# Kernel optimization log

Measured on AMD Instinct MI355X. Metric: run time of the kernel, lower is better.

The kernel has to match this reference:

```python
import jax, jax.numpy as jnp
import numpy as np

N, NDIM, K, M = 65536, 512, 512, 200


def setup_inputs() -> dict:
    key = jax.random.key(0)
    k1, k2, k3, k4, k5 = jax.random.split(key, 5)
    data = jax.random.normal(k1, (N, NDIM), dtype=jnp.float32)
    # Orthogonal projection A, as in __init__: QR of randn with sign fix
    A0 = np.asarray(jax.random.normal(k2, (NDIM, K), dtype=jnp.float32), dtype=np.float64)
    Q, R = np.linalg.qr(A0)
    A = jnp.asarray(Q * np.sign(np.diag(R)), dtype=jnp.float32)
    # Monotonic knot grids on roughly [-4, 4] with M knots per direction
    span = 8.0 / (M - 1)
    dx = jax.random.uniform(k3, (K, M - 1), minval=0.5 * span, maxval=1.5 * span)
    xx = jnp.concatenate([jnp.full((K, 1), -4.0), -4.0 + jnp.cumsum(dx, axis=1)], axis=1).astype(jnp.float32)
    dy = jax.random.uniform(k4, (K, M - 1), minval=0.5 * span, maxval=1.5 * span)
    yy = jnp.concatenate([jnp.full((K, 1), -4.0), -4.0 + jnp.cumsum(dy, axis=1)], axis=1).astype(jnp.float32)
    delta = jax.random.uniform(k5, (K, M), minval=0.5, maxval=2.0, dtype=jnp.float32)
    return {"data": data, "A": A, "xx": xx, "yy": yy, "delta": delta}


def _rq_spline_forward(x, xx, yy, delta):
    """Monotonic rational-quadratic spline, applied per dimension.
    x: (N, K) values; xx, yy, delta: (K, M) knot positions / values / derivatives.
    Returns (y, log|dy/dx|), both (N, K).
    """
    Mk = xx.shape[1]
    # Per-dimension bin search: idx in [0, Mk]
    idx = jax.vmap(jnp.searchsorted, in_axes=(0, 1))(xx, x).T  # (N, K)
    below = idx == 0
    above = idx == Mk
    b = jnp.clip(idx, 1, Mk - 1) - 1  # interior bin index, (N, K)
    bt = b.T  # (K, N) for take_along_axis on (K, M) tables
    g = lambda t, o: jnp.take_along_axis(t, bt + o, axis=1).T  # -> (N, K)
    xk, xk1 = g(xx, 0), g(xx, 1)
    yk, yk1 = g(yy, 0), g(yy, 1)
    dk, dk1 = g(delta, 0), g(delta, 1)
    dx = xk1 - xk
    dy = yk1 - yk
    s = dy / dx  # bin slope
    xi = jnp.clip((x - xk) / dx, 0.0, 1.0)  # clipped so out-of-range pts stay finite
    xi1 = 1.0 - xi
    denom = s + (dk1 + dk - 2.0 * s) * xi * xi1
    y_in = yk + dy * (s * xi * xi + dk * xi * xi1) / denom
    logd_in = (2.0 * jnp.log(s)
               + jnp.log(dk1 * xi * xi + 2.0 * s * xi * xi1 + dk * xi1 * xi1)
               - 2.0 * jnp.log(denom))
    # Linear extrapolation outside the knot range with endpoint derivatives
    x0, xN_ = xx[:, 0], xx[:, -1]
    y0, yN_ = yy[:, 0], yy[:, -1]
    d0, dN_ = delta[:, 0], delta[:, -1]
    y = jnp.where(below, y0 + d0 * (x - x0),
                  jnp.where(above, yN_ + dN_ * (x - xN_), y_in))
    logd = jnp.where(below, jnp.log(d0),
                     jnp.where(above, jnp.log(dN_), logd_in))
    return y, logd


def reference(data, A, xx, yy, delta):
    data0 = data @ A                    # (N, K) sliced projection
    remaining = data - data0 @ A.T      # component orthogonal to the slices
    y, logd = _rq_spline_forward(data0, xx, yy, delta)
    logj = jnp.sum(logd, axis=1)        # (N,) log-Jacobian
    out = remaining + y @ A.T
    return out, logj
```

## Files before the change

### kernel.cpp

```cpp
#include <hip/hip_runtime.h>

#define N_ROWS 65536
#define DIM 512
#define MKNOTS 200
#define KT 16
#define NCHUNK 2048
#define NCELL 768

typedef _Float16 f16x8 __attribute__((ext_vector_type(8)));
typedef _Float16 f16x4 __attribute__((ext_vector_type(4)));
typedef float f32x4 __attribute__((ext_vector_type(4)));

__device__ inline void gload16(const void* g, void* l) {
  __builtin_amdgcn_global_load_lds(
      (const __attribute__((address_space(1))) void*)g,
      (__attribute__((address_space(3))) void*)l,
      16, 0, 0);
}

template <bool S3, bool ADDSRC>
__global__ __launch_bounds__(256)
void gemm_k(const _Float16* __restrict__ Ah, const _Float16* __restrict__ Al,
            const _Float16* __restrict__ Bth, const _Float16* __restrict__ Btl,
            const float* __restrict__ addsrc, float* __restrict__ C)
{
  __shared__ alignas(16) _Float16 smem[S3 ? 16384 : 8192];
  _Float16* sAh = smem;
  _Float16* sBh = smem + 4096;
  _Float16* sAl = S3 ? smem + 8192  : smem;
  _Float16* sBl = S3 ? smem + 12288 : smem;

  const int tid  = threadIdx.x;
  const int bm   = blockIdx.x * 128;
  const int bn   = blockIdx.y * 128;
  const int wm   = ((tid >> 6) >> 1) * 64;
  const int wn   = ((tid >> 6) & 1) * 64;
  const int lane = tid & 63;
  const int lm   = lane & 15;
  const int quad = lane >> 4;
  const int sr   = tid >> 2;
  const int sc   = (tid & 3) * 8;

  const _Float16* gAh = Ah  + (size_t)(bm + sr) * DIM + sc;
  const _Float16* gBh = Bth + (size_t)(bn + sr) * DIM + sc;
  const _Float16* gAl = S3 ? (Al  + (size_t)(bm + sr) * DIM + sc) : gAh;
  const _Float16* gBl = S3 ? (Btl + (size_t)(bn + sr) * DIM + sc) : gBh;

  f32x4 acc[4][4] = {};

  for (int k0 = 0; k0 < DIM; k0 += 32) {
    gload16(gAh + k0,               sAh + tid * 8);
    gload16(gAh + k0 + 64 * DIM,    sAh + 2048 + tid * 8);
    gload16(gBh + k0,               sBh + tid * 8);
    gload16(gBh + k0 + 64 * DIM,    sBh + 2048 + tid * 8);
    if constexpr (S3) {
      gload16(gAl + k0,             sAl + tid * 8);
      gload16(gAl + k0 + 64 * DIM,  sAl + 2048 + tid * 8);
      gload16(gBl + k0,             sBl + tid * 8);
      gload16(gBl + k0 + 64 * DIM,  sBl + 2048 + tid * 8);
    }
    __syncthreads();

    f16x8 a_h[4], b_h[4], a_l[4], b_l[4];
    #pragma unroll
    for (int i = 0; i < 4; ++i) {
      a_h[i] = *(const f16x8*)&sAh[(wm + i * 16 + lm) * 32 + quad * 8];
      b_h[i] = *(const f16x8*)&sBh[(wn + i * 16 + lm) * 32 + quad * 8];
      if constexpr (S3) {
        a_l[i] = *(const f16x8*)&sAl[(wm + i * 16 + lm) * 32 + quad * 8];
        b_l[i] = *(const f16x8*)&sBl[(wn + i * 16 + lm) * 32 + quad * 8];
      }
    }
    #pragma unroll
    for (int i = 0; i < 4; ++i)
      #pragma unroll
      for (int j = 0; j < 4; ++j) {
        acc[i][j] = __builtin_amdgcn_mfma_f32_16x16x32_f16(a_h[i], b_h[j], acc[i][j], 0, 0, 0);
        if constexpr (S3) {
          acc[i][j] = __builtin_amdgcn_mfma_f32_16x16x32_f16(a_h[i], b_l[j], acc[i][j], 0, 0, 0);
          acc[i][j] = __builtin_amdgcn_mfma_f32_16x16x32_f16(a_l[i], b_h[j], acc[i][j], 0, 0, 0);
        }
      }
    __syncthreads();
  }

  #pragma unroll
  for (int i = 0; i < 4; ++i)
    #pragma unroll
    for (int j = 0; j < 4; ++j)
      #pragma unroll
      for (int r = 0; r < 4; ++r) {
        const int row = bm + wm + i * 16 + quad * 4 + r;
        const int col = bn + wn + j * 16 + lm;
        const size_t idx = (size_t)row * DIM + col;
        float v = acc[i][j][r];
        if constexpr (ADDSRC) v += addsrc[idx];
        C[idx] = v;
      }
}

__global__ __launch_bounds__(256)
void conv_data_k(const float* __restrict__ in, _Float16* __restrict__ hi,
                 _Float16* __restrict__ lo)
{
  const size_t i = ((size_t)blockIdx.x * 256 + threadIdx.x) * 4;
  const float4 v = *reinterpret_cast<const float4*>(in + i);
  f16x4 h, l;
  h.x = (_Float16)v.x; l.x = (_Float16)(v.x - (float)h.x);
  h.y = (_Float16)v.y; l.y = (_Float16)(v.y - (float)h.y);
  h.z = (_Float16)v.z; l.z = (_Float16)(v.z - (float)h.z);
  h.w = (_Float16)v.w; l.w = (_Float16)(v.w - (float)h.w);
  *reinterpret_cast<f16x4*>(hi + i) = h;
  *reinterpret_cast<f16x4*>(lo + i) = l;
}

__global__ __launch_bounds__(256)
void conv_A_k(const float* __restrict__ A, _Float16* __restrict__ Ah,
              _Float16* __restrict__ Al, _Float16* __restrict__ ATh,
              _Float16* __restrict__ ATl)
{
  const int i = blockIdx.x * 256 + threadIdx.x;
  const int r = i >> 9, c = i & 511;
  const float v = A[i];
  const _Float16 h = (_Float16)v;
  const _Float16 l = (_Float16)(v - (float)h);
  Ah[i] = h; Al[i] = l;
  ATh[c * 512 + r] = h; ATl[c * 512 + r] = l;
}

__global__ __launch_bounds__(256)
void prep_k(const float* __restrict__ xx, const float* __restrict__ yy,
            const float* __restrict__ dd, float4* __restrict__ pkG,
            unsigned char* __restrict__ bucketG)
{
  __shared__ float xr[MKNOTS], yr[MKNOTS];
  const int k = blockIdx.x, tid = threadIdx.x;
  if (tid < MKNOTS) {
    xr[tid] = xx[k * MKNOTS + tid];
    yr[tid] = yy[k * MKNOTS + tid];
  }
  __syncthreads();
  if (tid < MKNOTS) {
    const float x0 = xr[tid], y0 = yr[tid], d0 = dd[k * MKNOTS + tid];
    float s = 0.f;
    if (tid < MKNOTS - 1) s = (yr[tid + 1] - y0) / (xr[tid + 1] - x0);
    pkG[k * MKNOTS + tid] = float4{x0, y0, d0, s};
  }
  for (int c = tid; c < NCELL; c += 256) {
    const float cl = -4.f + (float)c * 0.015625f;
    int lo = 0, hi = MKNOTS;
    while (lo < hi) { const int mid = (lo + hi) >> 1; if (xr[mid] <= cl) lo = mid + 1; else hi = mid; }
    bucketG[k * NCELL + c] = (unsigned char)lo;
  }
}

__global__ __launch_bounds__(512)
void spline_k(const float* __restrict__ data0, const float4* __restrict__ pkG,
              const unsigned char* __restrict__ bucketG,
              _Float16* __restrict__ zH, float* __restrict__ logj)
{
  __shared__ float4 sPK[KT * (MKNOTS + 1)];
  __shared__ unsigned int sBkt32[KT * 193];

  const int kBase = blockIdx.x * KT;
  const int nBase = blockIdx.y * NCHUNK;
  const int tid = threadIdx.x;

  for (int i = tid; i < KT * MKNOTS; i += 512) {
    const int r = i / MKNOTS, c = i - r * MKNOTS;
    sPK[r * (MKNOTS + 1) + c] = pkG[(kBase + r) * MKNOTS + c];
  }
  const unsigned int* bG32 = (const unsigned int*)bucketG;
  for (int i = tid; i < KT * (NCELL / 4); i += 512) {
    const int r = i / (NCELL / 4), c = i - r * (NCELL / 4);
    sBkt32[r * 193 + c] = bG32[(kBase + r) * (NCELL / 4) + c];
  }
  __syncthreads();

  const int kl = tid & 15;
  const int nl = tid >> 4;
  const float4* prow = sPK + kl * (MKNOTS + 1);
  const unsigned char* brow = (const unsigned char*)sBkt32 + kl * 772;

  #pragma unroll 2
  for (int nn = nl; nn < NCHUNK; nn += 32) {
    const int n = nBase + nn;
    const size_t gi = (size_t)n * DIM + kBase + kl;
    const float x = data0[gi];

    int idx;
    if (x <= -4.f) {
      idx = 0;
    } else {
      int c = (int)((x + 4.f) * 64.f);
      c = min(c, NCELL - 1);
      const int cnt0 = (int)brow[c];
      const int p = min(cnt0, MKNOTS - 1);
      const float xp = ((const float*)(prow + p))[0];
      idx = cnt0 + ((cnt0 <= MKNOTS - 1 && xp < x) ? 1 : 0);
    }
    const bool below = (idx == 0);
    const bool above = (idx >= MKNOTS);
    const int b = min(max(idx - 1, 0), MKNOTS - 2);

    const float4 pa = prow[b];
    const float4 pb = prow[b + 1];

    const float dxk = pb.x - pa.x;
    float xi = (x - pa.x) * __builtin_amdgcn_rcpf(dxk);
    xi = fminf(fmaxf(xi, 0.f), 1.f);
    const float xi1 = 1.f - xi;
    const float t = pa.w;
    const float g = xi * xi1;
    const float den = t + (pb.z + pa.z - 2.f * t) * g;
    const float rden = __builtin_amdgcn_rcpf(den);
    const float ynum = t * xi * xi + pa.z * g;
    float y = pa.y + t * dxk * ynum * rden;
    const float dnum = pb.z * xi * xi + 2.f * t * g + pa.z * xi1 * xi1;
    float logd = __logf(t * t * dnum * rden * rden);

    if (below) { y = pa.y + pa.z * (x - pa.x); logd = __logf(pa.z); }
    if (above) { y = pb.y + pb.z * (x - pb.x); logd = __logf(pb.z); }

    zH[gi] = (_Float16)(y - x);

    float v = logd;
    v += __shfl_xor(v, 8, 64);
    v += __shfl_xor(v, 4, 64);
    v += __shfl_xor(v, 2, 64);
    v += __shfl_xor(v, 1, 64);
    if (kl == 0) atomicAdd(&logj[n], v);
  }
}

extern "C" void kernel_launch(void* const* d_in, const int* in_sizes, int n_in,
                              void* d_out, int out_size, void* d_ws, size_t ws_size,
                              hipStream_t stream)
{
  const float* data  = (const float*)d_in[0];
  const float* A     = (const float*)d_in[1];
  const float* xx    = (const float*)d_in[2];
  const float* yy    = (const float*)d_in[3];
  const float* delta = (const float*)d_in[4];

  float* out  = (float*)d_out;
  float* logj = out + (size_t)N_ROWS * DIM;

  _Float16* dHi = (_Float16*)d_ws;
  _Float16* dLo = dHi + (size_t)N_ROWS * DIM;
  _Float16* Ah  = dLo + (size_t)N_ROWS * DIM;
  _Float16* Al  = Ah + 512 * 512;
  _Float16* ATh = Al + 512 * 512;
  _Float16* ATl = ATh + 512 * 512;
  float* data0  = (float*)(ATl + 512 * 512);
  _Float16* zH  = dHi;
  float4* pkG = (float4*)dLo;
  unsigned char* bucketG = (unsigned char*)(pkG + 512 * MKNOTS);

  conv_A_k<<<1024, 256, 0, stream>>>(A, Ah, Al, ATh, ATl);
  conv_data_k<<<(N_ROWS * DIM) / (256 * 4), 256, 0, stream>>>(data, dHi, dLo);

  gemm_k<true, false><<<dim3(N_ROWS / 128, DIM / 128), 256, 0, stream>>>(
      dHi, dLo, ATh, ATl, nullptr, data0);

  prep_k<<<512, 256, 0, stream>>>(xx, yy, delta, pkG, bucketG);
  hipMemsetAsync(logj, 0, N_ROWS * sizeof(float), stream);

  spline_k<<<dim3(DIM / KT, N_ROWS / NCHUNK), 512, 0, stream>>>(
      data0, pkG, bucketG, zH, logj);

  gemm_k<false, true><<<dim3(N_ROWS / 128, DIM / 128), 256, 0, stream>>>(
      zH, nullptr, Ah, nullptr, data, out);
}
```

Before: 647.7 us.

## Restructure spline kernel to one thread per row with vector loads and prefetch

The spline kernel moves from 16 threads per row (one per dimension, with shuffle reductions) to one thread per row that handles 16 dimensions. It loads each row slice as four float4 vectors, prefetches the next row, writes the outputs as two f16x8 stores, and issues one atomic per row with no shuffles. The bin lookup is reworked so the probed knot is reused as one endpoint, and NCHUNK doubles. The aim is to cut scalar global accesses, shuffle reductions and atomics. The cost is higher register pressure, and each thread's 16 dimensions read from different shared-memory rows, which may cause bank conflicts.

```diff
diff --git a/kernel.cpp b/kernel.cpp
--- a/kernel.cpp
+++ b/kernel.cpp
@@ -4,7 +4,7 @@
 #define DIM 512
 #define MKNOTS 200
 #define KT 16
-#define NCHUNK 2048
+#define NCHUNK 4096
 #define NCELL 768
 
 typedef _Float16 f16x8 __attribute__((ext_vector_type(8)));
@@ -154,7 +154,7 @@
   }
 }
 
-__global__ __launch_bounds__(512)
+__global__ __launch_bounds__(512, 4)
 void spline_k(const float* __restrict__ data0, const float4* __restrict__ pkG,
               const unsigned char* __restrict__ bucketG,
               _Float16* __restrict__ zH, float* __restrict__ logj)
@@ -177,59 +177,72 @@
   }
   __syncthreads();
 
-  const int kl = tid & 15;
-  const int nl = tid >> 4;
-  const float4* prow = sPK + kl * (MKNOTS + 1);
-  const unsigned char* brow = (const unsigned char*)sBkt32 + kl * 772;
-
-  #pragma unroll 2
-  for (int nn = nl; nn < NCHUNK; nn += 32) {
-    const int n = nBase + nn;
-    const size_t gi = (size_t)n * DIM + kBase + kl;
-    const float x = data0[gi];
-
-    int idx;
-    if (x <= -4.f) {
-      idx = 0;
-    } else {
-      int c = (int)((x + 4.f) * 64.f);
-      c = min(c, NCELL - 1);
-      const int cnt0 = (int)brow[c];
+  float4 cur[4], nxt[4];
+  {
+    const float4* p4 = (const float4*)(data0 + (size_t)(nBase + tid) * DIM + kBase);
+    #pragma unroll
+    for (int q = 0; q < 4; ++q) cur[q] = p4[q];
+  }
+
+  for (int it = 0; it < NCHUNK / 512; ++it) {
+    const int n = nBase + it * 512 + tid;
+    if (it + 1 < NCHUNK / 512) {
+      const float4* p4 = (const float4*)(data0 + (size_t)(n + 512) * DIM + kBase);
+      #pragma unroll
+      for (int q = 0; q < 4; ++q) nxt[q] = p4[q];
+    }
+
+    float acc = 0.f;
+    f16x8 z0, z1;
+    #pragma unroll
+    for (int j = 0; j < 16; ++j) {
+      const float x = ((const float*)cur)[j];
+      const float4* prow = sPK + j * (MKNOTS + 1);
+      const unsigned char* brow = (const unsigned char*)sBkt32 + j * 772;
+
+      int cnt0 = 0;
+      if (x > -4.f) {
+        int c = (int)((x + 4.f) * 64.f);
+        c = min(c, NCELL - 1);
+        cnt0 = (int)brow[c];
+      }
       const int p = min(cnt0, MKNOTS - 1);
-      const float xp = ((const float*)(prow + p))[0];
-      idx = cnt0 + ((cnt0 <= MKNOTS - 1 && xp < x) ? 1 : 0);
-    }
-    const bool below = (idx == 0);
-    const bool above = (idx >= MKNOTS);
-    const int b = min(max(idx - 1, 0), MKNOTS - 2);
-
-    const float4 pa = prow[b];
-    const float4 pb = prow[b + 1];
-
-    const float dxk = pb.x - pa.x;
-    float xi = (x - pa.x) * __builtin_amdgcn_rcpf(dxk);
-    xi = fminf(fmaxf(xi, 0.f), 1.f);
-    const float xi1 = 1.f - xi;
-    const float t = pa.w;
-    const float g = xi * xi1;
-    const float den = t + (pb.z + pa.z - 2.f * t) * g;
-    const float rden = __builtin_amdgcn_rcpf(den);
-    const float ynum = t * xi * xi + pa.z * g;
-    float y = pa.y + t * dxk * ynum * rden;
-    const float dnum = pb.z * xi * xi + 2.f * t * g + pa.z * xi1 * xi1;
-    float logd = __logf(t * t * dnum * rden * rden);
-
-    if (below) { y = pa.y + pa.z * (x - pa.x); logd = __logf(pa.z); }
-    if (above) { y = pb.y + pb.z * (x - pb.x); logd = __logf(pb.z); }
-
-    zH[gi] = (_Float16)(y - x);
-
-    float v = logd;
-    v += __shfl_xor(v, 8, 64);
-    v += __shfl_xor(v, 4, 64);
-    v += __shfl_xor(v, 2, 64);
-    v += __shfl_xor(v, 1, 64);
-    if (kl == 0) atomicAdd(&logj[n], v);
+      const float4 P = prow[p];
+      const bool take = (cnt0 <= MKNOTS - 1) && (P.x < x);
+      const int idx = cnt0 + (take ? 1 : 0);
+      const int qi = min(max(take ? p + 1 : p - 1, 0), MKNOTS - 1);
+      const float4 Q = prow[qi];
+      const bool edge = (idx == 0) || (idx >= MKNOTS);
+      const float4 pa = take ? P : Q;
+      const float4 pb = take ? Q : P;
+
+      const float dxk = pb.x - pa.x;
+      float xi = (x - pa.x) * __builtin_amdgcn_rcpf(dxk);
+      xi = fminf(fmaxf(xi, 0.f), 1.f);
+      const float xi1 = 1.f - xi;
+      const float t = pa.w;
+      const float g = xi * xi1;
+      const float den = t + (pb.z + pa.z - 2.f * t) * g;
+      const float rden = __builtin_amdgcn_rcpf(den);
+      float y = pa.y + t * dxk * (t * xi * xi + pa.z * g) * rden;
+      const float dnum = pb.z * xi * xi + 2.f * t * g + pa.z * xi1 * xi1;
+      float logd = __logf(t * t * dnum * rden * rden);
+      if (edge) {
+        y = P.y + P.z * (x - P.x);
+        logd = __logf(P.z);
+      }
+      acc += logd;
+      const _Float16 zz = (_Float16)(y - x);
+      if (j < 8) z0[j] = zz; else z1[j - 8] = zz;
+    }
+
+    _Float16* zp = zH + (size_t)n * DIM + kBase;
+    *(f16x8*)zp = z0;
+    *((f16x8*)zp + 1) = z1;
+    atomicAdd(&logj[n], acc);
+
+    #pragma unroll
+    for (int q = 0; q < 4; ++q) cur[q] = nxt[q];
   }
 }
 
```

After: 798.8 us. 23.3% more time.

## Restructure spline kernel: transposed row tiles, SoA knot tables, partial-sum logj reduction

Applied to the files above, without the earlier changes.

The spline kernel now maps one thread per row. Each thread processes 16 dimensions from a tile staged in LDS, and the z results are packed as fp16 pairs and written back cooperatively in coalesced form. Knot tables move from float4 AoS to separate x/y arrays plus fp16 derivatives, and the bucket grid is coarsened to 384 cells with a 2-step linear refine. Per-row atomics on logj are replaced by per-k-group partial sums written to workspace and then summed by a new reduce kernel. Storing derivatives in fp16 reduces precision in the logd and y computation, and bucket lookups now read global memory instead of LDS.

```diff
diff --git a/kernel.cpp b/kernel.cpp
--- a/kernel.cpp
+++ b/kernel.cpp
@@ -4,8 +4,9 @@
 #define DIM 512
 #define MKNOTS 200
 #define KT 16
-#define NCHUNK 2048
-#define NCELL 768
+#define NCELL 384
+#define TILE 256
+#define TPB 4
 
 typedef _Float16 f16x8 __attribute__((ext_vector_type(8)));
 typedef _Float16 f16x4 __attribute__((ext_vector_type(4)));
@@ -147,90 +148,124 @@
     pkG[k * MKNOTS + tid] = float4{x0, y0, d0, s};
   }
   for (int c = tid; c < NCELL; c += 256) {
-    const float cl = -4.f + (float)c * 0.015625f;
+    const float cl = -4.f + (float)c * 0.03125f;
     int lo = 0, hi = MKNOTS;
     while (lo < hi) { const int mid = (lo + hi) >> 1; if (xr[mid] <= cl) lo = mid + 1; else hi = mid; }
     bucketG[k * NCELL + c] = (unsigned char)lo;
   }
 }
 
-__global__ __launch_bounds__(512)
+__global__ __launch_bounds__(256)
 void spline_k(const float* __restrict__ data0, const float4* __restrict__ pkG,
               const unsigned char* __restrict__ bucketG,
-              _Float16* __restrict__ zH, float* __restrict__ logj)
-{
-  __shared__ float4 sPK[KT * (MKNOTS + 1)];
-  __shared__ unsigned int sBkt32[KT * 193];
+              _Float16* __restrict__ zH, float* __restrict__ ppart)
+{
+  __shared__ float sX[KT * 201];
+  __shared__ float sY[KT * 201];
+  __shared__ _Float16 sD[KT * 201 + 2];
+  __shared__ float xT[TILE * 17];
 
   const int kBase = blockIdx.x * KT;
-  const int nBase = blockIdx.y * NCHUNK;
+  const int nBase = blockIdx.y * (TILE * TPB);
   const int tid = threadIdx.x;
 
-  for (int i = tid; i < KT * MKNOTS; i += 512) {
+  for (int i = tid; i < KT * MKNOTS; i += 256) {
     const int r = i / MKNOTS, c = i - r * MKNOTS;
-    sPK[r * (MKNOTS + 1) + c] = pkG[(kBase + r) * MKNOTS + c];
-  }
-  const unsigned int* bG32 = (const unsigned int*)bucketG;
-  for (int i = tid; i < KT * (NCELL / 4); i += 512) {
-    const int r = i / (NCELL / 4), c = i - r * (NCELL / 4);
-    sBkt32[r * 193 + c] = bG32[(kBase + r) * (NCELL / 4) + c];
+    const float4 v = pkG[(kBase + r) * MKNOTS + c];
+    sX[r * 201 + c] = v.x;
+    sY[r * 201 + c] = v.y;
+    sD[r * 201 + c] = (_Float16)v.z;
   }
   __syncthreads();
 
-  const int kl = tid & 15;
-  const int nl = tid >> 4;
-  const float4* prow = sPK + kl * (MKNOTS + 1);
-  const unsigned char* brow = (const unsigned char*)sBkt32 + kl * 772;
-
-  #pragma unroll 2
-  for (int nn = nl; nn < NCHUNK; nn += 32) {
-    const int n = nBase + nn;
-    const size_t gi = (size_t)n * DIM + kBase + kl;
-    const float x = data0[gi];
-
-    int idx;
-    if (x <= -4.f) {
-      idx = 0;
-    } else {
-      int c = (int)((x + 4.f) * 64.f);
-      c = min(c, NCELL - 1);
-      const int cnt0 = (int)brow[c];
-      const int p = min(cnt0, MKNOTS - 1);
-      const float xp = ((const float*)(prow + p))[0];
-      idx = cnt0 + ((cnt0 <= MKNOTS - 1 && xp < x) ? 1 : 0);
-    }
-    const bool below = (idx == 0);
-    const bool above = (idx >= MKNOTS);
-    const int b = min(max(idx - 1, 0), MKNOTS - 2);
-
-    const float4 pa = prow[b];
-    const float4 pb = prow[b + 1];
-
-    const float dxk = pb.x - pa.x;
-    float xi = (x - pa.x) * __builtin_amdgcn_rcpf(dxk);
-    xi = fminf(fmaxf(xi, 0.f), 1.f);
-    const float xi1 = 1.f - xi;
-    const float t = pa.w;
-    const float g = xi * xi1;
-    const float den = t + (pb.z + pa.z - 2.f * t) * g;
-    const float rden = __builtin_amdgcn_rcpf(den);
-    const float ynum = t * xi * xi + pa.z * g;
-    float y = pa.y + t * dxk * ynum * rden;
-    const float dnum = pb.z * xi * xi + 2.f * t * g + pa.z * xi1 * xi1;
-    float logd = __logf(t * t * dnum * rden * rden);
-
-    if (below) { y = pa.y + pa.z * (x - pa.x); logd = __logf(pa.z); }
-    if (above) { y = pb.y + pb.z * (x - pb.x); logd = __logf(pb.z); }
-
-    zH[gi] = (_Float16)(y - x);
-
-    float v = logd;
-    v += __shfl_xor(v, 8, 64);
-    v += __shfl_xor(v, 4, 64);
-    v += __shfl_xor(v, 2, 64);
-    v += __shfl_xor(v, 1, 64);
-    if (kl == 0) atomicAdd(&logj[n], v);
-  }
+  for (int tile = 0; tile < TPB; ++tile) {
+    const int n0 = nBase + tile * TILE;
+
+    #pragma unroll
+    for (int rr = 0; rr < 4; ++rr) {
+      const int r = rr * 64 + (tid >> 2);
+      const float4 v = *((const float4*)(data0 + (size_t)(n0 + r) * DIM + kBase) + (tid & 3));
+      float* dst = &xT[r * 17 + (tid & 3) * 4];
+      dst[0] = v.x; dst[1] = v.y; dst[2] = v.z; dst[3] = v.w;
+    }
+    __syncthreads();
+
+    float acc = 0.f;
+    float zprev = 0.f;
+    #pragma unroll 4
+    for (int j = 0; j < KT; ++j) {
+      const float x = xT[tid * 17 + j];
+
+      int c = (int)((x + 4.f) * 32.f);
+      c = min(max(c, 0), NCELL - 1);
+      const int cnt0 = (int)bucketG[(kBase + j) * NCELL + c];
+
+      const int p = min(cnt0, MKNOTS - 2);
+      const int q0 = p - 1;
+      const float* rx = &sX[j * 201];
+      const float xm = rx[q0], x0 = rx[q0 + 1], x1 = rx[q0 + 2], x2 = rx[q0 + 3];
+      const int t2 = (x0 < x ? 1 : 0) + (x1 < x ? 1 : 0);
+      const int idx = p + t2;
+      const bool below = (x <= -4.f);
+      const bool above = (idx >= MKNOTS);
+      const int b = idx - 1;
+
+      const float xk  = (t2 == 0) ? xm : ((t2 == 1) ? x0 : x1);
+      const float xk1 = (t2 == 0) ? x0 : ((t2 == 1) ? x1 : x2);
+      const float yk  = sY[j * 201 + b];
+      const float yk1 = sY[j * 201 + b + 1];
+      const float dk  = (float)sD[j * 201 + b];
+      const float dk1 = (float)sD[j * 201 + b + 1];
+
+      const float dxk = xk1 - xk;
+      const float rdx = __builtin_amdgcn_rcpf(dxk);
+      const float s   = (yk1 - yk) * rdx;
+      float xi = (x - xk) * rdx;
+      xi = fminf(fmaxf(xi, 0.f), 1.f);
+      const float xi1 = 1.f - xi;
+      const float g = xi * xi1;
+      const float den = s + (dk1 + dk - 2.f * s) * g;
+      const float rden = __builtin_amdgcn_rcpf(den);
+      const float y_in = yk + s * dxk * (s * xi * xi + dk * g) * rden;
+      const float dnum = dk1 * xi * xi + 2.f * s * g + dk * xi1 * xi1;
+      const float ld_in = __logf(s * s * dnum * rden * rden);
+
+      const bool edge = below || above;
+      const float y  = edge ? (yk + dk * (x - xk)) : y_in;
+      const float ld = edge ? __logf(dk) : ld_in;
+      acc += ld;
+
+      const float z = y - x;
+      if (j & 1) {
+        union { _Float16 h[2]; unsigned int u; } pk2;
+        pk2.h[0] = (_Float16)zprev; pk2.h[1] = (_Float16)z;
+        ((unsigned int*)xT)[tid * 17 + (j >> 1)] = pk2.u;
+      } else {
+        zprev = z;
+      }
+    }
+    ppart[(size_t)blockIdx.x * N_ROWS + n0 + tid] = acc;
+    __syncthreads();
+
+    const int w = tid & 7;
+    #pragma unroll
+    for (int ri = 0; ri < 8; ++ri) {
+      const int r = ri * 32 + (tid >> 3);
+      const unsigned int zz = ((const unsigned int*)xT)[r * 17 + w];
+      *(unsigned int*)(zH + (size_t)(n0 + r) * DIM + kBase + w * 2) = zz;
+    }
+    __syncthreads();
+  }
+}
+
+__global__ __launch_bounds__(256)
+void reduce_k(const float* __restrict__ ppart, float* __restrict__ logj)
+{
+  const int n = blockIdx.x * 256 + threadIdx.x;
+  float a = 0.f;
+  #pragma unroll
+  for (int t = 0; t < 32; ++t) a += ppart[(size_t)t * N_ROWS + n];
+  logj[n] = a;
 }
 
 extern "C" void kernel_launch(void* const* d_in, const int* in_sizes, int n_in,
@@ -256,6 +291,7 @@
   _Float16* zH  = dHi;
   float4* pkG = (float4*)dLo;
   unsigned char* bucketG = (unsigned char*)(pkG + 512 * MKNOTS);
+  float* ppart = (float*)(bucketG + 512 * NCELL);
 
   conv_A_k<<<1024, 256, 0, stream>>>(A, Ah, Al, ATh, ATl);
   conv_data_k<<<(N_ROWS * DIM) / (256 * 4), 256, 0, stream>>>(data, dHi, dLo);
@@ -264,10 +300,11 @@
       dHi, dLo, ATh, ATl, nullptr, data0);
 
   prep_k<<<512, 256, 0, stream>>>(xx, yy, delta, pkG, bucketG);
-  hipMemsetAsync(logj, 0, N_ROWS * sizeof(float), stream);
-
-  spline_k<<<dim3(DIM / KT, N_ROWS / NCHUNK), 512, 0, stream>>>(
-      data0, pkG, bucketG, zH, logj);
+
+  spline_k<<<dim3(DIM / KT, N_ROWS / (TILE * TPB)), 256, 0, stream>>>(
+      data0, pkG, bucketG, zH, ppart);
+
+  reduce_k<<<N_ROWS / 256, 256, 0, stream>>>(ppart, logj);
 
   gemm_k<false, true><<<dim3(N_ROWS / 128, DIM / 128), 256, 0, stream>>>(
       zH, nullptr, Ah, nullptr, data, out);
```

Result: faster. 607.3 us (-6.2%).
